# Kernel optimization log

Measured on AMD Instinct MI355X. Metric: run time of the kernel, lower is better.

Reference implementation:

```python
import jax, jax.numpy as jnp
import numpy as np

NUM_USER = 100000
NUM_ITEM = 50000
N = NUM_USER + NUM_ITEM
E = 1200000
D = 64          # emb_size
F_ITEM = 384    # raw item multimodal feature dim
K = 3           # number of global embedding rows (summed over dim 0)
N_LAYERS = 4
EPS = 1e-8      # F.cosine_similarity default eps


def setup_inputs() -> dict:
    key = jax.random.key(0)
    ks = jax.random.split(key, 9)
    return {
        "adj_row": jax.random.randint(ks[0], (E,), 0, N),
        "adj_col": jax.random.randint(ks[1], (E,), 0, N),
        # scaled like a degree-normalized adjacency (avg degree ~8)
        "adj_val": jax.random.uniform(ks[2], (E,), jnp.float32) / 8.0,
        "user_fea": jax.random.normal(ks[3], (NUM_USER, D), jnp.float32) * 0.1,
        "item_fea": jax.random.normal(ks[4], (NUM_ITEM, F_ITEM), jnp.float32) * 0.1,
        "g_emb_u": jax.random.normal(ks[5], (K, D), jnp.float32) * 0.1,
        "g_emb_i": jax.random.normal(ks[6], (K, D), jnp.float32) * 0.1,
        "mlp_w": jax.random.normal(ks[7], (D, F_ITEM), jnp.float32) * (1.0 / np.sqrt(F_ITEM)),
        "mlp_b": jnp.zeros((D,), jnp.float32),
    }


def _cosine_sim(a, b):
    # matches F.cosine_similarity(a, b, dim=-1) with eps clamp on norms
    na = jnp.maximum(jnp.linalg.norm(a, axis=-1), EPS)
    nb = jnp.maximum(jnp.linalg.norm(b, axis=-1), EPS)
    return jnp.sum(a * b, axis=-1) / (na * nb)


def reference(adj_row, adj_col, adj_val, user_fea, item_fea, g_emb_u, g_emb_i, mlp_w, mlp_b):
    # global embeddings summed over modality dim
    user_emb = user_fea + jnp.sum(g_emb_u, axis=0)                       # [U, D]
    item_emb = jnp.tanh(item_fea @ mlp_w.T + mlp_b) + jnp.sum(g_emb_i, axis=0)  # [I, D]
    ego = jnp.concatenate([user_emb, item_emb], axis=0)                  # [N, D]

    x = ego
    acc = ego  # sum over layers, includes layer-0 (ego) term
    for _ in range(N_LAYERS):
        # sparse adj @ x as gather -> scale -> segment-sum scatter
        x = jax.ops.segment_sum(adj_val[:, None] * x[adj_col], adj_row, num_segments=N)
        w = _cosine_sim(x, ego)     # [N]
        x = w[:, None] * x          # einsum('a,ab->ab')
        acc = acc + x

    return acc[:NUM_USER], acc[NUM_USER:]
```

## Files before the change

kernel.cpp:

```cpp
#include <hip/hip_runtime.h>
#include <hip/hip_bf16.h>

#define U_NUM 100000
#define I_NUM 50000
#define N_NUM 150000
#define E_NUM 1200000
#define D 64
#define F_IT 384
#define CAP 32
#define EPSV 1e-8f
#define FXS 524288.0f
#define FXI (1.0f / 524288.0f)

#define NBIN 586
#define RPB 256
#define FBLK 586
#define CELL_CAP 8
#define OV_CAP 256

typedef unsigned short ushort_t;
typedef unsigned int uint_t;
typedef short bf16x8 __attribute__((ext_vector_type(8)));
typedef float f32x4 __attribute__((ext_vector_type(4)));

__device__ __forceinline__ ushort_t f2bf(float f) {
    uint_t x = __float_as_uint(f);
    uint_t r = x + 0x7fffu + ((x >> 16) & 1u);
    return (ushort_t)(r >> 16);
}
__device__ __forceinline__ float bfu2f(uint_t u_lo16) {
    return __uint_as_float(u_lo16 << 16);
}
__device__ __forceinline__ void dec8(uint4 u, float* f) {
    f[0] = bfu2f(u.x & 0xffffu); f[1] = bfu2f(u.x >> 16);
    f[2] = bfu2f(u.y & 0xffffu); f[3] = bfu2f(u.y >> 16);
    f[4] = bfu2f(u.z & 0xffffu); f[5] = bfu2f(u.z >> 16);
    f[6] = bfu2f(u.w & 0xffffu); f[7] = bfu2f(u.w >> 16);
}

__global__ void k_prep(const float* __restrict__ w, const float* __restrict__ gu,
                       const float* __restrict__ gi,
                       short* __restrict__ wbf, float* __restrict__ gsu,
                       float* __restrict__ gsi, int* __restrict__ ovcnt) {
    int b = blockIdx.x, t = threadIdx.x;
    if (b < 96) {
        int i = b * 256 + t;
        wbf[i] = (short)f2bf(w[i]);
    } else {
        if (t < 64) gsu[t] = gu[t] + gu[64 + t] + gu[128 + t];
        else if (t < 128) { int d = t - 64; gsi[d] = gi[d] + gi[64 + d] + gi[128 + d]; }
        for (int i = t; i < NBIN; i += 256) ovcnt[i] = 0;
    }
}

__global__ __launch_bounds__(256) void k_fill(
        const int* __restrict__ row, const int* __restrict__ col,
        const float* __restrict__ val,
        int2* __restrict__ cellbuf, int* __restrict__ cellcnt,
        int* __restrict__ ovcnt, int2* __restrict__ ovbuf) {
    __shared__ int bincnt[NBIN];
    int fid = blockIdx.x, tid = threadIdx.x;
    for (int i = tid; i < NBIN; i += 256) bincnt[i] = 0;
    __syncthreads();
    int t = fid * 256 + tid;
    if (t < E_NUM / 8) {
        int r[8], c[8];
        float v[8];
#pragma unroll
        for (int k = 0; k < 8; k++) {
            int e = k * (E_NUM / 8) + t;
            r[k] = row[e]; c[k] = col[e]; v[k] = val[e];
        }
#pragma unroll
        for (int k = 0; k < 8; k++) {
            int bn = r[k] >> 8;
            int key = c[k] | ((r[k] & 255) << 18);
            int ls = atomicAdd(&bincnt[bn], 1);
            if (ls < CELL_CAP) {
                cellbuf[((size_t)fid * NBIN + bn) * CELL_CAP + ls] =
                    make_int2(key, __float_as_int(v[k]));
            } else {
                int o = atomicAdd(&ovcnt[bn], 1);
                if (o < OV_CAP) ovbuf[bn * OV_CAP + o] = make_int2(key, __float_as_int(v[k]));
            }
        }
    }
    __syncthreads();
    for (int i = tid; i < NBIN; i += 256)
        cellcnt[(size_t)fid * NBIN + i] = min(bincnt[i], CELL_CAP);
}

#define ITEM_B 782
__global__ __launch_bounds__(256) void k_item(
        const float* __restrict__ ifea, const float* __restrict__ bvec,
        const short* __restrict__ wbf, const float* __restrict__ gsi,
        float* __restrict__ ego, ushort_t* __restrict__ egob) {
    int iid = blockIdx.x;
    int tid = threadIdx.x;
    int wave = tid >> 6, lane = tid & 63;
    int q = lane >> 4, m = lane & 15;
    int ibase = iid * 64 + wave * 16;
    int irow = min(ibase + m, I_NUM - 1);
    const float* arow = ifea + (size_t)irow * F_IT + q * 8;

    f32x4 av[4];
#pragma unroll
    for (int n = 0; n < 4; n++) av[n] = (f32x4){0.f, 0.f, 0.f, 0.f};
    float4 nfa0 = ((const float4*)(arow))[0];
    float4 nfa1 = ((const float4*)(arow))[1];
#pragma unroll
    for (int c = 0; c < 12; c++) {
        float4 fa0 = nfa0, fa1 = nfa1;
        if (c < 11) {
            nfa0 = ((const float4*)(arow + (c + 1) * 32))[0];
            nfa1 = ((const float4*)(arow + (c + 1) * 32))[1];
        }
        bf16x8 af;
        af[0] = (short)f2bf(fa0.x); af[1] = (short)f2bf(fa0.y);
        af[2] = (short)f2bf(fa0.z); af[3] = (short)f2bf(fa0.w);
        af[4] = (short)f2bf(fa1.x); af[5] = (short)f2bf(fa1.y);
        af[6] = (short)f2bf(fa1.z); af[7] = (short)f2bf(fa1.w);
#pragma unroll
        for (int n = 0; n < 4; n++) {
            bf16x8 bf = *(const bf16x8*)(wbf + (size_t)(n * 16 + m) * F_IT + c * 32 + q * 8);
            av[n] = __builtin_amdgcn_mfma_f32_16x16x32_bf16(af, bf, av[n], 0, 0, 0);
        }
    }
#pragma unroll
    for (int n = 0; n < 4; n++) {
        int dim = n * 16 + m;
        float bb = bvec[dim];
        float gg = gsi[dim];
#pragma unroll
        for (int rr = 0; rr < 4; rr++) {
            int item = ibase + q * 4 + rr;
            if (item < I_NUM) {
                float v = tanhf(av[n][rr] + bb) + gg;
                size_t o = (size_t)(U_NUM + item) * D + dim;
                ego[o] = v;
                egob[o] = f2bf(v);
            }
        }
    }
}

#define USER_B 1563
__global__ __launch_bounds__(256) void k_user(
        const float* __restrict__ ufea, const float* __restrict__ gsu,
        float* __restrict__ ego, ushort_t* __restrict__ egob) {
    int t = blockIdx.x * 256 + threadIdx.x;
    size_t base = (size_t)t * 16;
    if (base >= (size_t)U_NUM * D) return;
    int d0 = (int)(base & 63);
    float f[16];
#pragma unroll
    for (int k = 0; k < 4; k++) {
        float4 v = ((const float4*)(ufea + base))[k];
        f[4 * k] = v.x; f[4 * k + 1] = v.y; f[4 * k + 2] = v.z; f[4 * k + 3] = v.w;
    }
#pragma unroll
    for (int j = 0; j < 16; j++) f[j] += gsu[d0 + j];
#pragma unroll
    for (int k = 0; k < 4; k++) {
        ((float4*)(ego + base))[k] = make_float4(f[4 * k], f[4 * k + 1], f[4 * k + 2], f[4 * k + 3]);
    }
    uint4 u0, u1;
    u0.x = (uint_t)f2bf(f[0]) | ((uint_t)f2bf(f[1]) << 16);
    u0.y = (uint_t)f2bf(f[2]) | ((uint_t)f2bf(f[3]) << 16);
    u0.z = (uint_t)f2bf(f[4]) | ((uint_t)f2bf(f[5]) << 16);
    u0.w = (uint_t)f2bf(f[6]) | ((uint_t)f2bf(f[7]) << 16);
    u1.x = (uint_t)f2bf(f[8]) | ((uint_t)f2bf(f[9]) << 16);
    u1.y = (uint_t)f2bf(f[10]) | ((uint_t)f2bf(f[11]) << 16);
    u1.z = (uint_t)f2bf(f[12]) | ((uint_t)f2bf(f[13]) << 16);
    u1.w = (uint_t)f2bf(f[14]) | ((uint_t)f2bf(f[15]) << 16);
    ((uint4*)(egob + base))[0] = u0;
    ((uint4*)(egob + base))[1] = u1;
}

__global__ __launch_bounds__(256) void k_bucket(const int2* __restrict__ cellbuf,
                                                const int* __restrict__ cellcnt,
                                                const int* __restrict__ ovcnt,
                                                const int2* __restrict__ ovbuf,
                                                int* __restrict__ cnt,
                                                int2* __restrict__ bkt) {
    __shared__ int lc[RPB];
    int bn = blockIdx.x, tid = threadIdx.x;
    lc[tid] = 0;
    __syncthreads();
    int rbase = bn << 8;
#pragma unroll
    for (int h = 0; h < 3; h++) {
        int f = h * 256 + tid;
        if (f < FBLK) {
            int c = cellcnt[(size_t)f * NBIN + bn];
            const int2* cp = cellbuf + ((size_t)f * NBIN + bn) * CELL_CAP;
            for (int i = 0; i < c; i++) {
                int2 e = cp[i];
                int rl = e.x >> 18;
                int s = atomicAdd(&lc[rl], 1);
                if (s < CAP) bkt[(size_t)(rbase + rl) * CAP + s] = make_int2(e.x & 0x3ffff, e.y);
            }
        }
    }
    int oc = min(ovcnt[bn], OV_CAP);
    for (int i = tid; i < oc; i += 256) {
        int2 e = ovbuf[bn * OV_CAP + i];
        int rl = e.x >> 18;
        int s = atomicAdd(&lc[rl], 1);
        if (s < CAP) bkt[(size_t)(rbase + rl) * CAP + s] = make_int2(e.x & 0x3ffff, e.y);
    }
    __syncthreads();
    int r = rbase + tid;
    if (r < N_NUM) {
        int d = min(lc[tid], CAP);
        int dp = (d + 7) & ~7;
        for (int s = d; s < dp; s++)
            bkt[(size_t)r * CAP + s] = make_int2(0, 0);
        cnt[r] = dp;
    }
}

#define ACC8(A, VS, X) \
    A[0] += __float2int_rn(VS * bfu2f(X.x & 0xffffu)); A[1] += __float2int_rn(VS * bfu2f(X.x >> 16)); \
    A[2] += __float2int_rn(VS * bfu2f(X.y & 0xffffu)); A[3] += __float2int_rn(VS * bfu2f(X.y >> 16)); \
    A[4] += __float2int_rn(VS * bfu2f(X.z & 0xffffu)); A[5] += __float2int_rn(VS * bfu2f(X.z >> 16)); \
    A[6] += __float2int_rn(VS * bfu2f(X.w & 0xffffu)); A[7] += __float2int_rn(VS * bfu2f(X.w >> 16));

__device__ __forceinline__ float row_weight(const float* a, const float* e) {
    float dot = 0.f, nx = 0.f, ne = 0.f;
#pragma unroll
    for (int j = 0; j < 8; j++) {
        dot += a[j] * e[j]; nx += a[j] * a[j]; ne += e[j] * e[j];
    }
#pragma unroll
    for (int m = 1; m < 8; m <<= 1) {
        dot += __shfl_xor(dot, m);
        nx  += __shfl_xor(nx, m);
        ne  += __shfl_xor(ne, m);
    }
    return dot / (fmaxf(sqrtf(nx), EPSV) * fmaxf(sqrtf(ne), EPSV));
}

__device__ __forceinline__ void gather_row(const ushort_t* __restrict__ xb,
                                           const int2* __restrict__ bp,
                                           int nch, int l, int* __restrict__ a) {
#pragma unroll
    for (int j = 0; j < 8; j++) a[j] = 0;
    const int4* cp = (const int4*)bp;
#pragma unroll
    for (int k = 0; k < 4; k++) {
        if (k < nch) {
            int4 p01 = cp[4 * k + 0];
            int4 p23 = cp[4 * k + 1];
            int4 p45 = cp[4 * k + 2];
            int4 p67 = cp[4 * k + 3];
            uint4 xu[8];
            xu[0] = ((const uint4*)xb)[(size_t)p01.x * 8 + l];
            xu[1] = ((const uint4*)xb)[(size_t)p01.z * 8 + l];
            xu[2] = ((const uint4*)xb)[(size_t)p23.x * 8 + l];
            xu[3] = ((const uint4*)xb)[(size_t)p23.z * 8 + l];
            xu[4] = ((const uint4*)xb)[(size_t)p45.x * 8 + l];
            xu[5] = ((const uint4*)xb)[(size_t)p45.z * 8 + l];
            xu[6] = ((const uint4*)xb)[(size_t)p67.x * 8 + l];
            xu[7] = ((const uint4*)xb)[(size_t)p67.z * 8 + l];
            float vs0 = __int_as_float(p01.y) * FXS, vs1 = __int_as_float(p01.w) * FXS;
            float vs2 = __int_as_float(p23.y) * FXS, vs3 = __int_as_float(p23.w) * FXS;
            float vs4 = __int_as_float(p45.y) * FXS, vs5 = __int_as_float(p45.w) * FXS;
            float vs6 = __int_as_float(p67.y) * FXS, vs7 = __int_as_float(p67.w) * FXS;
            ACC8(a, vs0, xu[0]); ACC8(a, vs1, xu[1]);
            ACC8(a, vs2, xu[2]); ACC8(a, vs3, xu[3]);
            ACC8(a, vs4, xu[4]); ACC8(a, vs5, xu[5]);
            ACC8(a, vs6, xu[6]); ACC8(a, vs7, xu[7]);
        }
    }
}

__device__ __forceinline__ void spmm_body(const ushort_t* __restrict__ xb,
                                          const ushort_t* __restrict__ egob,
                                          const int* __restrict__ cnt,
                                          const int2* __restrict__ bkt,
                                          ushort_t* __restrict__ xob) {
    int t = blockIdx.x * 256 + threadIdx.x;
    int l = t & 7, r = t >> 3;
    if (r >= N_NUM) return;
    int nch = cnt[r] >> 3;
    int a[8];
    gather_row(xb, bkt + (size_t)r * CAP, nch, l, a);
    float af[8];
#pragma unroll
    for (int j = 0; j < 8; j++) af[j] = (float)a[j] * FXI;
    float e[8]; dec8(((const uint4*)egob)[(size_t)r * 8 + l], e);
    float wgt = row_weight(af, e);
    uint4 ov;
    ov.x = (uint_t)f2bf(wgt * af[0]) | ((uint_t)f2bf(wgt * af[1]) << 16);
    ov.y = (uint_t)f2bf(wgt * af[2]) | ((uint_t)f2bf(wgt * af[3]) << 16);
    ov.z = (uint_t)f2bf(wgt * af[4]) | ((uint_t)f2bf(wgt * af[5]) << 16);
    ov.w = (uint_t)f2bf(wgt * af[6]) | ((uint_t)f2bf(wgt * af[7]) << 16);
    ((uint4*)xob)[(size_t)r * 8 + l] = ov;
}

__global__ __launch_bounds__(256, 5) void k_spmmA(const ushort_t* __restrict__ xb,
        const ushort_t* __restrict__ egob, const int* __restrict__ cnt,
        const int2* __restrict__ bkt, ushort_t* __restrict__ xob)
{ spmm_body(xb, egob, cnt, bkt, xob); }

__global__ __launch_bounds__(256, 5) void k_spmmB(const ushort_t* __restrict__ xb,
        const ushort_t* __restrict__ egob, const int* __restrict__ cnt,
        const int2* __restrict__ bkt, ushort_t* __restrict__ xob)
{ spmm_body(xb, egob, cnt, bkt, xob); }

__global__ __launch_bounds__(256, 5) void k_spmmC(const ushort_t* __restrict__ xb,
        const ushort_t* __restrict__ egob, const int* __restrict__ cnt,
        const int2* __restrict__ bkt, ushort_t* __restrict__ xob)
{ spmm_body(xb, egob, cnt, bkt, xob); }

__global__ __launch_bounds__(256, 5) void k_spmm4(const ushort_t* __restrict__ x3,
                                                  const ushort_t* __restrict__ x1,
                                                  const ushort_t* __restrict__ x2,
                                                  const float* __restrict__ ego,
                                                  const int* __restrict__ cnt,
                                                  const int2* __restrict__ bkt,
                                                  float* __restrict__ out) {
    int t = blockIdx.x * 256 + threadIdx.x;
    int l = t & 7, r = t >> 3;
    if (r >= N_NUM) return;
    int nch = cnt[r] >> 3;
    int a[8];
    gather_row(x3, bkt + (size_t)r * CAP, nch, l, a);
    float af[8];
#pragma unroll
    for (int j = 0; j < 8; j++) af[j] = (float)a[j] * FXI;
    size_t rb = (size_t)r * D + l * 8;
    float e[8];
    float4 e0 = ((const float4*)(ego + rb))[0];
    float4 e1 = ((const float4*)(ego + rb))[1];
    e[0] = e0.x; e[1] = e0.y; e[2] = e0.z; e[3] = e0.w;
    e[4] = e1.x; e[5] = e1.y; e[6] = e1.z; e[7] = e1.w;
    float wgt = row_weight(af, e);
    float x1d[8], x2d[8], x3d[8];
    dec8(((const uint4*)x1)[(size_t)r * 8 + l], x1d);
    dec8(((const uint4*)x2)[(size_t)r * 8 + l], x2d);
    dec8(((const uint4*)x3)[(size_t)r * 8 + l], x3d);
    float s[8];
#pragma unroll
    for (int j = 0; j < 8; j++) s[j] = e[j] + x1d[j] + x2d[j] + x3d[j] + wgt * af[j];
    ((float4*)(out + rb))[0] = make_float4(s[0], s[1], s[2], s[3]);
    ((float4*)(out + rb))[1] = make_float4(s[4], s[5], s[6], s[7]);
}

extern "C" void kernel_launch(void* const* d_in, const int* in_sizes, int n_in,
                              void* d_out, int out_size, void* d_ws, size_t ws_size,
                              hipStream_t stream) {
    const int*   adj_row  = (const int*)d_in[0];
    const int*   adj_col  = (const int*)d_in[1];
    const float* adj_val  = (const float*)d_in[2];
    const float* user_fea = (const float*)d_in[3];
    const float* item_fea = (const float*)d_in[4];
    const float* gu       = (const float*)d_in[5];
    const float* gi       = (const float*)d_in[6];
    const float* mlp_w    = (const float*)d_in[7];
    const float* mlp_b    = (const float*)d_in[8];

    float* out = (float*)d_out;

    char* ws = (char*)d_ws;
    size_t off = 0;
    float*    ego  = (float*)(ws + off);    off += (size_t)N_NUM * D * 4;
    ushort_t* egob = (ushort_t*)(ws + off); off += (size_t)N_NUM * D * 2;
    size_t x1off = off;
    ushort_t* x1   = (ushort_t*)(ws + off); off += (size_t)N_NUM * D * 2;
    ushort_t* x2   = (ushort_t*)(ws + off); off += (size_t)N_NUM * D * 2;
    ushort_t* x3   = (ushort_t*)(ws + off); off += (size_t)N_NUM * D * 2;
    int*      cnt  = (int*)(ws + off);      off += (size_t)N_NUM * 4;
    short*    wbf  = (short*)(ws + off);    off += (size_t)D * F_IT * 2;
    float*    gsu  = (float*)(ws + off);    off += 64 * 4;
    float*    gsi  = (float*)(ws + off);    off += 64 * 4;
    off = (off + 255) & ~(size_t)255;
    int2*     bkt  = (int2*)(ws + off);     off += (size_t)N_NUM * CAP * 8;
    int*      cellcnt = (int*)(ws + off);   off += (size_t)FBLK * NBIN * 4;
    int*      ovcnt   = (int*)(ws + off);   off += (size_t)NBIN * 4;
    int2*     ovbuf   = (int2*)(ws + off);  off += (size_t)NBIN * OV_CAP * 8;
    int2*     cellbuf = (int2*)(ws + x1off);

    k_prep<<<97, 256, 0, stream>>>(mlp_w, gu, gi, wbf, gsu, gsi, ovcnt);
    k_fill<<<FBLK, 256, 0, stream>>>(adj_row, adj_col, adj_val,
                                     cellbuf, cellcnt, ovcnt, ovbuf);
    k_item<<<ITEM_B, 256, 0, stream>>>(item_fea, mlp_b, wbf, gsi, ego, egob);
    k_user<<<USER_B, 256, 0, stream>>>(user_fea, gsu, ego, egob);
    k_bucket<<<NBIN, 256, 0, stream>>>(cellbuf, cellcnt, ovcnt, ovbuf, cnt, bkt);
    int g = ((size_t)N_NUM * 8 + 255) / 256;
    k_spmmA<<<g, 256, 0, stream>>>(egob, egob, cnt, bkt, x1);
    k_spmmB<<<g, 256, 0, stream>>>(x1,   egob, cnt, bkt, x2);
    k_spmmC<<<g, 256, 0, stream>>>(x2,   egob, cnt, bkt, x3);
    k_spmm4<<<g, 256, 0, stream>>>(x3, x1, x2, ego, cnt, bkt, out);
}
```

Before: 398.4 us.

## Use 16 lanes per row with 8-byte gathers and 16/32-edge padding

The SpMM kernels now map each row to 16 threads holding 4 features each, instead of 8 threads holding 8, so the per-edge gather is an 8-byte load rather than a 16-byte one. Bucket padding is coarsened to 16 or 32 slots, which lets the gather issue 16 neighbor loads at once with no per-chunk branching. The min-waves launch bound is dropped. This doubles the thread count and memory-level parallelism but adds padded zero-edge work (the average degree is about 8, so most rows pad to 16) and a longer shuffle reduction.

```diff
diff --git a/kernel.cpp b/kernel.cpp
--- a/kernel.cpp
+++ b/kernel.cpp
@@ -31,11 +31,9 @@
 __device__ __forceinline__ float bfu2f(uint_t u_lo16) {
     return __uint_as_float(u_lo16 << 16);
 }
-__device__ __forceinline__ void dec8(uint4 u, float* f) {
+__device__ __forceinline__ void dec4(uint2 u, float* f) {
     f[0] = bfu2f(u.x & 0xffffu); f[1] = bfu2f(u.x >> 16);
     f[2] = bfu2f(u.y & 0xffffu); f[3] = bfu2f(u.y >> 16);
-    f[4] = bfu2f(u.z & 0xffffu); f[5] = bfu2f(u.z >> 16);
-    f[6] = bfu2f(u.w & 0xffffu); f[7] = bfu2f(u.w >> 16);
 }
 
 __global__ void k_prep(const float* __restrict__ w, const float* __restrict__ gu,
@@ -213,27 +211,25 @@
     int r = rbase + tid;
     if (r < N_NUM) {
         int d = min(lc[tid], CAP);
-        int dp = (d + 7) & ~7;
+        int dp = (d <= 16) ? 16 : 32;
         for (int s = d; s < dp; s++)
             bkt[(size_t)r * CAP + s] = make_int2(0, 0);
         cnt[r] = dp;
     }
 }
 
-#define ACC8(A, VS, X) \
+#define ACC4(A, VS, X) \
     A[0] += __float2int_rn(VS * bfu2f(X.x & 0xffffu)); A[1] += __float2int_rn(VS * bfu2f(X.x >> 16)); \
-    A[2] += __float2int_rn(VS * bfu2f(X.y & 0xffffu)); A[3] += __float2int_rn(VS * bfu2f(X.y >> 16)); \
-    A[4] += __float2int_rn(VS * bfu2f(X.z & 0xffffu)); A[5] += __float2int_rn(VS * bfu2f(X.z >> 16)); \
-    A[6] += __float2int_rn(VS * bfu2f(X.w & 0xffffu)); A[7] += __float2int_rn(VS * bfu2f(X.w >> 16));
-
-__device__ __forceinline__ float row_weight(const float* a, const float* e) {
+    A[2] += __float2int_rn(VS * bfu2f(X.y & 0xffffu)); A[3] += __float2int_rn(VS * bfu2f(X.y >> 16));
+
+__device__ __forceinline__ float row_weight16(const float* a, const float* e) {
     float dot = 0.f, nx = 0.f, ne = 0.f;
 #pragma unroll
-    for (int j = 0; j < 8; j++) {
+    for (int j = 0; j < 4; j++) {
         dot += a[j] * e[j]; nx += a[j] * a[j]; ne += e[j] * e[j];
     }
 #pragma unroll
-    for (int m = 1; m < 8; m <<= 1) {
+    for (int m = 1; m < 16; m <<= 1) {
         dot += __shfl_xor(dot, m);
         nx  += __shfl_xor(nx, m);
         ne  += __shfl_xor(ne, m);
@@ -241,37 +237,24 @@
     return dot / (fmaxf(sqrtf(nx), EPSV) * fmaxf(sqrtf(ne), EPSV));
 }
 
-__device__ __forceinline__ void gather_row(const ushort_t* __restrict__ xb,
-                                           const int2* __restrict__ bp,
-                                           int nch, int l, int* __restrict__ a) {
-#pragma unroll
-    for (int j = 0; j < 8; j++) a[j] = 0;
-    const int4* cp = (const int4*)bp;
-#pragma unroll
-    for (int k = 0; k < 4; k++) {
-        if (k < nch) {
-            int4 p01 = cp[4 * k + 0];
-            int4 p23 = cp[4 * k + 1];
-            int4 p45 = cp[4 * k + 2];
-            int4 p67 = cp[4 * k + 3];
-            uint4 xu[8];
-            xu[0] = ((const uint4*)xb)[(size_t)p01.x * 8 + l];
-            xu[1] = ((const uint4*)xb)[(size_t)p01.z * 8 + l];
-            xu[2] = ((const uint4*)xb)[(size_t)p23.x * 8 + l];
-            xu[3] = ((const uint4*)xb)[(size_t)p23.z * 8 + l];
-            xu[4] = ((const uint4*)xb)[(size_t)p45.x * 8 + l];
-            xu[5] = ((const uint4*)xb)[(size_t)p45.z * 8 + l];
-            xu[6] = ((const uint4*)xb)[(size_t)p67.x * 8 + l];
-            xu[7] = ((const uint4*)xb)[(size_t)p67.z * 8 + l];
-            float vs0 = __int_as_float(p01.y) * FXS, vs1 = __int_as_float(p01.w) * FXS;
-            float vs2 = __int_as_float(p23.y) * FXS, vs3 = __int_as_float(p23.w) * FXS;
-            float vs4 = __int_as_float(p45.y) * FXS, vs5 = __int_as_float(p45.w) * FXS;
-            float vs6 = __int_as_float(p67.y) * FXS, vs7 = __int_as_float(p67.w) * FXS;
-            ACC8(a, vs0, xu[0]); ACC8(a, vs1, xu[1]);
-            ACC8(a, vs2, xu[2]); ACC8(a, vs3, xu[3]);
-            ACC8(a, vs4, xu[4]); ACC8(a, vs5, xu[5]);
-            ACC8(a, vs6, xu[6]); ACC8(a, vs7, xu[7]);
-        }
+__device__ __forceinline__ void gather16(const ushort_t* __restrict__ xb,
+                                         const int4* __restrict__ cp, int l,
+                                         int* __restrict__ a) {
+    int4 p[8];
+#pragma unroll
+    for (int j = 0; j < 8; j++) p[j] = cp[j];
+    uint2 xu[16];
+#pragma unroll
+    for (int j = 0; j < 8; j++) {
+        xu[2 * j]     = ((const uint2*)xb)[(size_t)p[j].x * 16 + l];
+        xu[2 * j + 1] = ((const uint2*)xb)[(size_t)p[j].z * 16 + l];
+    }
+#pragma unroll
+    for (int j = 0; j < 8; j++) {
+        float va = __int_as_float(p[j].y) * FXS;
+        float vb = __int_as_float(p[j].w) * FXS;
+        ACC4(a, va, xu[2 * j]);
+        ACC4(a, vb, xu[2 * j + 1]);
     }
 }
 
@@ -281,71 +264,68 @@
                                           const int2* __restrict__ bkt,
                                           ushort_t* __restrict__ xob) {
     int t = blockIdx.x * 256 + threadIdx.x;
-    int l = t & 7, r = t >> 3;
+    int l = t & 15, r = t >> 4;
     if (r >= N_NUM) return;
-    int nch = cnt[r] >> 3;
-    int a[8];
-    gather_row(xb, bkt + (size_t)r * CAP, nch, l, a);
-    float af[8];
-#pragma unroll
-    for (int j = 0; j < 8; j++) af[j] = (float)a[j] * FXI;
-    float e[8]; dec8(((const uint4*)egob)[(size_t)r * 8 + l], e);
-    float wgt = row_weight(af, e);
-    uint4 ov;
+    int dp = cnt[r];
+    const int4* cp = (const int4*)(bkt + (size_t)r * CAP);
+    int a[4] = {0, 0, 0, 0};
+    gather16(xb, cp, l, a);
+    if (dp > 16) gather16(xb, cp + 8, l, a);
+    float af[4];
+#pragma unroll
+    for (int j = 0; j < 4; j++) af[j] = (float)a[j] * FXI;
+    float e[4]; dec4(((const uint2*)egob)[(size_t)r * 16 + l], e);
+    float wgt = row_weight16(af, e);
+    uint2 ov;
     ov.x = (uint_t)f2bf(wgt * af[0]) | ((uint_t)f2bf(wgt * af[1]) << 16);
     ov.y = (uint_t)f2bf(wgt * af[2]) | ((uint_t)f2bf(wgt * af[3]) << 16);
-    ov.z = (uint_t)f2bf(wgt * af[4]) | ((uint_t)f2bf(wgt * af[5]) << 16);
-    ov.w = (uint_t)f2bf(wgt * af[6]) | ((uint_t)f2bf(wgt * af[7]) << 16);
-    ((uint4*)xob)[(size_t)r * 8 + l] = ov;
-}
-
-__global__ __launch_bounds__(256, 5) void k_spmmA(const ushort_t* __restrict__ xb,
+    ((uint2*)xob)[(size_t)r * 16 + l] = ov;
+}
+
+__global__ __launch_bounds__(256) void k_spmmA(const ushort_t* __restrict__ xb,
         const ushort_t* __restrict__ egob, const int* __restrict__ cnt,
         const int2* __restrict__ bkt, ushort_t* __restrict__ xob)
 { spmm_body(xb, egob, cnt, bkt, xob); }
 
-__global__ __launch_bounds__(256, 5) void k_spmmB(const ushort_t* __restrict__ xb,
+__global__ __launch_bounds__(256) void k_spmmB(const ushort_t* __restrict__ xb,
         const ushort_t* __restrict__ egob, const int* __restrict__ cnt,
         const int2* __restrict__ bkt, ushort_t* __restrict__ xob)
 { spmm_body(xb, egob, cnt, bkt, xob); }
 
-__global__ __launch_bounds__(256, 5) void k_spmmC(const ushort_t* __restrict__ xb,
+__global__ __launch_bounds__(256) void k_spmmC(const ushort_t* __restrict__ xb,
         const ushort_t* __restrict__ egob, const int* __restrict__ cnt,
         const int2* __restrict__ bkt, ushort_t* __restrict__ xob)
 { spmm_body(xb, egob, cnt, bkt, xob); }
 
-__global__ __launch_bounds__(256, 5) void k_spmm4(const ushort_t* __restrict__ x3,
-                                                  const ushort_t* __restrict__ x1,
-                                                  const ushort_t* __restrict__ x2,
-                                                  const float* __restrict__ ego,
-                                                  const int* __restrict__ cnt,
-                                                  const int2* __restrict__ bkt,
-                                                  float* __restrict__ out) {
+__global__ __launch_bounds__(256) void k_spmm4(const ushort_t* __restrict__ x3,
+                                               const ushort_t* __restrict__ x1,
+                                               const ushort_t* __restrict__ x2,
+                                               const float* __restrict__ ego,
+                                               const int* __restrict__ cnt,
+                                               const int2* __restrict__ bkt,
+                                               float* __restrict__ out) {
     int t = blockIdx.x * 256 + threadIdx.x;
-    int l = t & 7, r = t >> 3;
+    int l = t & 15, r = t >> 4;
     if (r >= N_NUM) return;
-    int nch = cnt[r] >> 3;
-    int a[8];
-    gather_row(x3, bkt + (size_t)r * CAP, nch, l, a);
-    float af[8];
-#pragma unroll
-    for (int j = 0; j < 8; j++) af[j] = (float)a[j] * FXI;
-    size_t rb = (size_t)r * D + l * 8;
-    float e[8];
-    float4 e0 = ((const float4*)(ego + rb))[0];
-    float4 e1 = ((const float4*)(ego + rb))[1];
-    e[0] = e0.x; e[1] = e0.y; e[2] = e0.z; e[3] = e0.w;
-    e[4] = e1.x; e[5] = e1.y; e[6] = e1.z; e[7] = e1.w;
-    float wgt = row_weight(af, e);
-    float x1d[8], x2d[8], x3d[8];
-    dec8(((const uint4*)x1)[(size_t)r * 8 + l], x1d);
-    dec8(((const uint4*)x2)[(size_t)r * 8 + l], x2d);
-    dec8(((const uint4*)x3)[(size_t)r * 8 + l], x3d);
-    float s[8];
-#pragma unroll
-    for (int j = 0; j < 8; j++) s[j] = e[j] + x1d[j] + x2d[j] + x3d[j] + wgt * af[j];
-    ((float4*)(out + rb))[0] = make_float4(s[0], s[1], s[2], s[3]);
-    ((float4*)(out + rb))[1] = make_float4(s[4], s[5], s[6], s[7]);
+    int dp = cnt[r];
+    const int4* cp = (const int4*)(bkt + (size_t)r * CAP);
+    int a[4] = {0, 0, 0, 0};
+    gather16(x3, cp, l, a);
+    if (dp > 16) gather16(x3, cp + 8, l, a);
+    float af[4];
+#pragma unroll
+    for (int j = 0; j < 4; j++) af[j] = (float)a[j] * FXI;
+    float4 ev = ((const float4*)ego)[(size_t)r * 16 + l];
+    float e[4] = {ev.x, ev.y, ev.z, ev.w};
+    float wgt = row_weight16(af, e);
+    float x1d[4], x2d[4], x3d[4];
+    dec4(((const uint2*)x1)[(size_t)r * 16 + l], x1d);
+    dec4(((const uint2*)x2)[(size_t)r * 16 + l], x2d);
+    dec4(((const uint2*)x3)[(size_t)r * 16 + l], x3d);
+    float s[4];
+#pragma unroll
+    for (int j = 0; j < 4; j++) s[j] = e[j] + x1d[j] + x2d[j] + x3d[j] + wgt * af[j];
+    ((float4*)out)[(size_t)r * 16 + l] = make_float4(s[0], s[1], s[2], s[3]);
 }
 
 extern "C" void kernel_launch(void* const* d_in, const int* in_sizes, int n_in,
@@ -388,9 +368,9 @@
     k_item<<<ITEM_B, 256, 0, stream>>>(item_fea, mlp_b, wbf, gsi, ego, egob);
     k_user<<<USER_B, 256, 0, stream>>>(user_fea, gsu, ego, egob);
     k_bucket<<<NBIN, 256, 0, stream>>>(cellbuf, cellcnt, ovcnt, ovbuf, cnt, bkt);
-    int g = ((size_t)N_NUM * 8 + 255) / 256;
-    k_spmmA<<<g, 256, 0, stream>>>(egob, egob, cnt, bkt, x1);
-    k_spmmB<<<g, 256, 0, stream>>>(x1,   egob, cnt, bkt, x2);
-    k_spmmC<<<g, 256, 0, stream>>>(x2,   egob, cnt, bkt, x3);
-    k_spmm4<<<g, 256, 0, stream>>>(x3, x1, x2, ego, cnt, bkt, out);
-}
+    int g16 = ((size_t)N_NUM * 16 + 255) / 256;
+    k_spmmA<<<g16, 256, 0, stream>>>(egob, egob, cnt, bkt, x1);
+    k_spmmB<<<g16, 256, 0, stream>>>(x1,   egob, cnt, bkt, x2);
+    k_spmmC<<<g16, 256, 0, stream>>>(x2,   egob, cnt, bkt, x3);
+    k_spmm4<<<g16, 256, 0, stream>>>(x3, x1, x2, ego, cnt, bkt, out);
+}
```

Measured after the change: 394.3 us. About the same (-1.0%).
